# Kernel tuning notes

Hardware: AMD Instinct MI355X
Metric: run time of the kernel (lower is better)

Reference implementation:

```python
import jax, jax.numpy as jnp
import numpy as np

NUM_EMBEDDINGS = 1024
EMBEDDING_DIM = 256
COMMITMENT_COST = 0.25


def setup_inputs() -> dict:
    key = jax.random.key(0)
    k1, k2 = jax.random.split(key)
    inputs = jax.random.normal(k1, (64, 32, 32, EMBEDDING_DIM), dtype=jnp.float32)
    embed = jax.random.normal(k2, (NUM_EMBEDDINGS, EMBEDDING_DIM), dtype=jnp.float32)
    return {"inputs": inputs, "embed": embed}


def reference(inputs, embed):
    # Eval-mode forward (no EMA buffer mutation), use_ema=True loss branch.
    input_shape = inputs.shape
    flat = inputs.reshape(-1, EMBEDDING_DIM)  # [N, d]
    distances = (
        jnp.sum(flat * flat, axis=1, keepdims=True)
        + jnp.sum(embed * embed, axis=1)
        - 2.0 * jnp.matmul(flat, embed.T)
    )
    encoding_indices = jnp.argmin(distances, axis=1)  # [N]
    # Gather codebook rows (equivalent to one-hot @ embed)
    quantized = embed[encoding_indices].reshape(input_shape)
    # use_ema branch: loss = commitment * mse(stop_grad(quantized), inputs)
    e_latent_loss = jnp.mean((jax.lax.stop_gradient(quantized) - inputs) ** 2)
    loss = COMMITMENT_COST * e_latent_loss
    # Straight-through estimator
    quantized_st = inputs + jax.lax.stop_gradient(quantized - inputs)
    # Perplexity from code usage histogram (== mean of one-hot encodings)
    n_tokens = flat.shape[0]
    counts = jax.ops.segment_sum(
        jnp.ones((n_tokens,), dtype=jnp.float32), encoding_indices,
        num_segments=NUM_EMBEDDINGS)
    avg_probs = counts / n_tokens
    perplexity = jnp.exp(-jnp.sum(avg_probs * jnp.log(avg_probs + 1e-10)))
    return quantized_st, loss, perplexity, encoding_indices
```

## Files before the change

### kernel.cpp

```cpp
#include <hip/hip_runtime.h>

#define NTOK 65536
#define DIM 256
#define KC 1024
#define EPS 0.08f

typedef __attribute__((ext_vector_type(8))) _Float16 f16x8;
typedef __attribute__((ext_vector_type(4))) float f32x4;

static __device__ __forceinline__ unsigned short f16bits(float f) {
  _Float16 h = (_Float16)f;
  return __builtin_bit_cast(unsigned short, h);
}
static __device__ __forceinline__ void gload16(const void* g, void* l) {
  __builtin_amdgcn_global_load_lds(
      (const __attribute__((address_space(1))) unsigned int*)g,
      (__attribute__((address_space(3))) unsigned int*)l, 16, 0, 0);
}

__global__ __launch_bounds__(256) void vq_prep_e(const float* __restrict__ e,
                                                 unsigned short* __restrict__ eg,
                                                 float* __restrict__ esq,
                                                 int* __restrict__ hist,
                                                 int* __restrict__ fixCount) {
  const int w = threadIdx.x >> 6, l = threadIdx.x & 63;
  const int t = blockIdx.x * 4 + w;
  const float4 v = *reinterpret_cast<const float4*>(&e[t * DIM + l * 4]);
  ushort4 o;
  o.x = f16bits(v.x); o.y = f16bits(v.y); o.z = f16bits(v.z); o.w = f16bits(v.w);
  const int addr = t * 512 + ((l >> 4) << 7) + ((((l & 15) * 8) ^ ((t & 7) << 4)));
  *reinterpret_cast<ushort4*>((char*)eg + addr) = o;
  float s = v.x * v.x + v.y * v.y + v.z * v.z + v.w * v.w;
#pragma unroll
  for (int o2 = 32; o2 > 0; o2 >>= 1) s += __shfl_down(s, o2, 64);
  if (l == 0) esq[t] = s;
  if (blockIdx.x < 4) hist[blockIdx.x * 256 + threadIdx.x] = 0;
  if (blockIdx.x == 0 && threadIdx.x == 0) *fixCount = 0;
}

__global__ __launch_bounds__(256, 2) void vq_argmin_fused(
    const float* __restrict__ x, const unsigned short* __restrict__ eg,
    const float* __restrict__ e, const float* __restrict__ esq,
    float* __restrict__ outIdxF, float* __restrict__ outQ,
    float* __restrict__ bestDist, float* __restrict__ xsq,
    int* __restrict__ hist, int* __restrict__ fixCount,
    int* __restrict__ fixList) {
  __shared__ unsigned short xs[128 * 256];
  __shared__ unsigned short es[128 * 64];

  const int tid = threadIdx.x, lane = tid & 63, w = tid >> 6;
  const int wr = w >> 1, wc = w & 1;
  const int tokBase = blockIdx.x * 128;
  const int col = lane & 15, kq = lane >> 4;

  {
    const float4* xb = reinterpret_cast<const float4*>(&x[tokBase * DIM]);
    for (int c = 0; c < 32; ++c) {
      const int r = c * 4 + w;
      const float4 v = xb[c * 256 + tid];
      ushort4 o;
      o.x = f16bits(v.x); o.y = f16bits(v.y); o.z = f16bits(v.z); o.w = f16bits(v.w);
      const int addr =
          r * 512 + ((lane >> 4) << 7) + ((((lane & 15) * 8) ^ ((r & 7) << 4)));
      *reinterpret_cast<ushort4*>((char*)xs + addr) = o;
      float s = v.x * v.x + v.y * v.y + v.z * v.z + v.w * v.w;
#pragma unroll
      for (int o2 = 32; o2 > 0; o2 >>= 1) s += __shfl_down(s, o2, 64);
      if (lane == 0) xsq[tokBase + r] = s;
    }
  }

  float best[4][4], second[4][4];
  int bidx[4][4];
#pragma unroll
  for (int mi = 0; mi < 4; ++mi)
#pragma unroll
    for (int r = 0; r < 4; ++r) {
      best[mi][r] = 3.4e38f; second[mi][r] = 3.4e38f; bidx[mi][r] = 0;
    }

  for (int ct = 0; ct < 8; ++ct) {
    f32x4 acc[4][4];
#pragma unroll
    for (int mi = 0; mi < 4; ++mi)
#pragma unroll
      for (int nj = 0; nj < 4; ++nj) acc[mi][nj] = (f32x4){0.f, 0.f, 0.f, 0.f};

    for (int kt = 0; kt < 4; ++kt) {
      __syncthreads();
#pragma unroll
      for (int q = 0; q < 4; ++q) {
        const int r0 = (w * 4 + q) * 8;
        const int er = ct * 128 + r0 + (lane >> 3);
        gload16(&eg[er * DIM + kt * 64 + (lane & 7) * 8], &es[r0 * 64]);
      }
      __syncthreads();

#pragma unroll
      for (int ks = 0; ks < 2; ++ks) {
        const int kb = ks * 64 + kq * 16;
        f16x8 a[4], b[4];
#pragma unroll
        for (int mi = 0; mi < 4; ++mi) {
          const int rr = wr * 64 + mi * 16 + col;
          a[mi] = *reinterpret_cast<const f16x8*>(
              (const char*)xs + rr * 512 + kt * 128 + (kb ^ ((col & 7) << 4)));
        }
#pragma unroll
        for (int nj = 0; nj < 4; ++nj) {
          const int rr = wc * 64 + nj * 16 + col;
          b[nj] = *reinterpret_cast<const f16x8*>(
              (const char*)es + rr * 128 + (kb ^ ((col & 7) << 4)));
        }
#pragma unroll
        for (int mi = 0; mi < 4; ++mi)
#pragma unroll
          for (int nj = 0; nj < 4; ++nj)
            acc[mi][nj] = __builtin_amdgcn_mfma_f32_16x16x32_f16(
                a[mi], b[nj], acc[mi][nj], 0, 0, 0);
      }
    }

#pragma unroll
    for (int nj = 0; nj < 4; ++nj) {
      const int code = ct * 128 + wc * 64 + nj * 16 + col;
      const float sqv = esq[code];
#pragma unroll
      for (int mi = 0; mi < 4; ++mi)
#pragma unroll
        for (int r = 0; r < 4; ++r) {
          const float d = fmaf(-2.f, acc[mi][nj][r], sqv);
          if (d < best[mi][r]) {
            second[mi][r] = best[mi][r];
            best[mi][r] = d;
            bidx[mi][r] = code;
          } else if (d < second[mi][r]) {
            second[mi][r] = d;
          }
        }
    }
  }

  __syncthreads();
  float* redB = (float*)es;
  float* redS = redB + 256;
  int*   redI = (int*)(redS + 256);
  int*   fIdx = redI + 256;

#pragma unroll
  for (int mi = 0; mi < 4; ++mi)
#pragma unroll
    for (int r = 0; r < 4; ++r) {
      float b = best[mi][r], s2 = second[mi][r];
      int bi = bidx[mi][r];
#pragma unroll
      for (int m = 1; m <= 8; m <<= 1) {
        const float ob = __shfl_xor(b, m, 64);
        const float os = __shfl_xor(s2, m, 64);
        const int   oi = __shfl_xor(bi, m, 64);
        s2 = fminf(fminf(s2, os), fmaxf(b, ob));
        if (ob < b || (ob == b && oi < bi)) { b = ob; bi = oi; }
      }
      if (col == 0) {
        const int row = wr * 64 + mi * 16 + kq * 4 + r;
        redB[wc * 128 + row] = b; redS[wc * 128 + row] = s2;
        redI[wc * 128 + row] = bi;
      }
    }
  __syncthreads();
  if (tid < 128) {
    const float b0 = redB[tid], b1 = redB[128 + tid];
    const float s0 = redS[tid], s1 = redS[128 + tid];
    const int i0 = redI[tid], i1 = redI[128 + tid];
    const float s2 = fminf(fminf(s0, s1), fmaxf(b0, b1));
    float b; int bi;
    if (b1 < b0 || (b1 == b0 && i1 < i0)) { b = b1; bi = i1; } else { b = b0; bi = i0; }
    const int t = tokBase + tid;
    outIdxF[t] = (float)bi;
    bestDist[t] = b;
    fIdx[tid] = bi;
    atomicAdd(&hist[bi], 1);
    if (s2 - b < EPS) {
      const int p = atomicAdd(fixCount, 1);
      fixList[p] = t;
    }
  }
  __syncthreads();

  for (int i = 0; i < 32; ++i) {
    const int tl = w * 32 + i;
    const int id = fIdx[tl];
    const float4 q = reinterpret_cast<const float4*>(&e[id * DIM])[lane];
    reinterpret_cast<float4*>(&outQ[(tokBase + tl) * DIM])[lane] = q;
  }
}

__global__ __launch_bounds__(256) void vq_fixup(
    const float* __restrict__ x, const float* __restrict__ e,
    const float* __restrict__ esq, const int* __restrict__ fixCount,
    const int* __restrict__ fixList, float* __restrict__ outIdxF,
    float* __restrict__ bestDist, float* __restrict__ outQ,
    int* __restrict__ hist) {
  const int n = *fixCount;
  __shared__ float xrow[256];
  __shared__ float rv[4];
  __shared__ int ri[4];
  __shared__ int sOld, sFi;
  const int tid = threadIdx.x;
  for (int it = blockIdx.x; it < n; it += gridDim.x) {
    const int t = fixList[it];
    __syncthreads();
    if (tid < 64) ((float4*)xrow)[tid] = ((const float4*)&x[t * DIM])[tid];
    __syncthreads();
    float bv = 3.4e38f; int bi = 0;
    for (int c = tid; c < KC; c += 256) {
      float s = 0.f;
#pragma unroll
      for (int d = 0; d < DIM; d += 4) {
        const float4 ev = *(const float4*)&e[c * DIM + d];
        s = fmaf(xrow[d], ev.x, s);
        s = fmaf(xrow[d + 1], ev.y, s);
        s = fmaf(xrow[d + 2], ev.z, s);
        s = fmaf(xrow[d + 3], ev.w, s);
      }
      const float dist = fmaf(-2.f, s, esq[c]);
      if (dist < bv) { bv = dist; bi = c; }
    }
#pragma unroll
    for (int m = 1; m <= 32; m <<= 1) {
      const float ob = __shfl_xor(bv, m, 64);
      const int oi = __shfl_xor(bi, m, 64);
      if (ob < bv || (ob == bv && oi < bi)) { bv = ob; bi = oi; }
    }
    const int lane = tid & 63, wv = tid >> 6;
    if (lane == 0) { rv[wv] = bv; ri[wv] = bi; }
    __syncthreads();
    if (tid == 0) {
      float fb = rv[0]; int fi = ri[0];
      for (int k = 1; k < 4; ++k)
        if (rv[k] < fb || (rv[k] == fb && ri[k] < fi)) { fb = rv[k]; fi = ri[k]; }
      sOld = (int)outIdxF[t];
      sFi = fi;
      bestDist[t] = fb;
      if (fi != sOld) {
        atomicSub(&hist[sOld], 1);
        atomicAdd(&hist[fi], 1);
        outIdxF[t] = (float)fi;
      }
    }
    __syncthreads();
    if (sFi != sOld) outQ[t * DIM + tid] = e[sFi * DIM + tid];
    __syncthreads();
  }
}

__global__ __launch_bounds__(1024) void vq_final(
    const int* __restrict__ hist, const float* __restrict__ xsq,
    const float* __restrict__ bestDist, float* __restrict__ outLoss,
    float* __restrict__ outPerp) {
  const int tid = threadIdx.x;
  float ls = 0.f;
  for (int i = 0; i < 64; ++i) {
    const int t = tid + i * 1024;
    ls += xsq[t] + bestDist[t];
  }
  const float p = (float)hist[tid] * (1.f / 65536.f);
  float ent = p * logf(p + 1e-10f);
#pragma unroll
  for (int o = 32; o > 0; o >>= 1) {
    ls += __shfl_down(ls, o, 64);
    ent += __shfl_down(ent, o, 64);
  }
  __shared__ float lbuf[16], ebuf[16];
  const int lane = tid & 63, wv = tid >> 6;
  if (lane == 0) { lbuf[wv] = ls; ebuf[wv] = ent; }
  __syncthreads();
  if (tid == 0) {
    float L = 0.f, E = 0.f;
    for (int i = 0; i < 16; ++i) { L += lbuf[i]; E += ebuf[i]; }
    *outLoss = 0.25f * (L / 16777216.f);
    *outPerp = expf(-E);
  }
}

extern "C" void kernel_launch(void* const* d_in, const int* in_sizes, int n_in,
                              void* d_out, int out_size, void* d_ws, size_t ws_size,
                              hipStream_t stream) {
  const float* x = (const float*)d_in[0];
  const float* e = (const float*)d_in[1];
  float* out = (float*)d_out;
  float* outQ = out;
  float* outLoss = out + 16777216;
  float* outPerp = out + 16777217;
  float* outIdxF = out + 16777218;

  char* ws = (char*)d_ws;
  int*   hist     = (int*)ws;
  float* esq      = (float*)(ws + 4096);
  float* xsq      = (float*)(ws + 8192);
  float* bestDist = (float*)(ws + 270336);
  int*   fixCount = (int*)(ws + 532480);
  int*   fixList  = (int*)(ws + 532496);
  unsigned short* e_f16 = (unsigned short*)(ws + 794640);

  vq_prep_e<<<KC / 4, 256, 0, stream>>>(e, e_f16, esq, hist, fixCount);
  vq_argmin_fused<<<NTOK / 128, 256, 0, stream>>>(
      x, e_f16, e, esq, outIdxF, outQ, bestDist, xsq, hist, fixCount, fixList);
  vq_fixup<<<256, 256, 0, stream>>>(x, e, esq, fixCount, fixList, outIdxF,
                                    bestDist, outQ, hist);
  vq_final<<<1, 1024, 0, stream>>>(hist, xsq, bestDist, outLoss, outPerp);
}
```

Measured before the change: 204.7 us.

## Keep token fragments in registers and triple-buffer codebook tiles with async loads

Each wave now owns 32 tokens across all 128 codes per tile and holds its fp16 A-fragments in registers, loaded straight from global memory. This removes the 64KB shared-memory x tile and the cross-wave argmin reduction. Codebook tiles are triple-buffered in LDS with global_load_lds prefetch of the next tile, using vmcnt waits and one barrier per tile instead of two syncthreads. The cost is much higher register pressure (64 VGPRs of A fragments plus 32 accumulators), which could lower occupancy or cause spills under launch_bounds(256,2). The uncoalesced per-lane x loads also replace the previous coalesced staging.

New measurement: 198.0 us. 1.03x faster.

```diff
diff --git a/kernel.cpp b/kernel.cpp
--- a/kernel.cpp
+++ b/kernel.cpp
@@ -45,88 +45,105 @@
     float* __restrict__ bestDist, float* __restrict__ xsq,
     int* __restrict__ hist, int* __restrict__ fixCount,
     int* __restrict__ fixList) {
-  __shared__ unsigned short xs[128 * 256];
-  __shared__ unsigned short es[128 * 64];
+  __shared__ unsigned short es[3 * 8192];
+  __shared__ int fidx[128];
 
   const int tid = threadIdx.x, lane = tid & 63, w = tid >> 6;
-  const int wr = w >> 1, wc = w & 1;
   const int tokBase = blockIdx.x * 128;
   const int col = lane & 15, kq = lane >> 4;
 
-  {
-    const float4* xb = reinterpret_cast<const float4*>(&x[tokBase * DIM]);
-    for (int c = 0; c < 32; ++c) {
-      const int r = c * 4 + w;
-      const float4 v = xb[c * 256 + tid];
-      ushort4 o;
-      o.x = f16bits(v.x); o.y = f16bits(v.y); o.z = f16bits(v.z); o.w = f16bits(v.w);
-      const int addr =
-          r * 512 + ((lane >> 4) << 7) + ((((lane & 15) * 8) ^ ((r & 7) << 4)));
-      *reinterpret_cast<ushort4*>((char*)xs + addr) = o;
-      float s = v.x * v.x + v.y * v.y + v.z * v.z + v.w * v.w;
-#pragma unroll
-      for (int o2 = 32; o2 > 0; o2 >>= 1) s += __shfl_down(s, o2, 64);
-      if (lane == 0) xsq[tokBase + r] = s;
-    }
-  }
-
-  float best[4][4], second[4][4];
-  int bidx[4][4];
-#pragma unroll
-  for (int mi = 0; mi < 4; ++mi)
+  auto STAGE = [&](int tile, int b) {
+    const int ct_ = tile >> 2, kt_ = tile & 3;
+#pragma unroll
+    for (int q = 0; q < 4; ++q) {
+      const int r0 = w * 32 + q * 8;
+      const int er = ct_ * 128 + r0 + (lane >> 3);
+      gload16(&eg[er * DIM + kt_ * 64 + (lane & 7) * 8], &es[b * 8192 + r0 * 64]);
+    }
+  };
+
+  STAGE(0, 0);
+
+  f16x8 a[2][8];
+  float sqm[2] = {0.f, 0.f};
+#pragma unroll
+  for (int m = 0; m < 2; ++m) {
+#pragma unroll
+    for (int s = 0; s < 8; ++s) {
+      const float* xp =
+          &x[(tokBase + w * 32 + m * 16 + col) * DIM + s * 32 + kq * 8];
+      const float4 v0 = *reinterpret_cast<const float4*>(xp);
+      const float4 v1 = *reinterpret_cast<const float4*>(xp + 4);
+      a[m][s][0] = (_Float16)v0.x; a[m][s][1] = (_Float16)v0.y;
+      a[m][s][2] = (_Float16)v0.z; a[m][s][3] = (_Float16)v0.w;
+      a[m][s][4] = (_Float16)v1.x; a[m][s][5] = (_Float16)v1.y;
+      a[m][s][6] = (_Float16)v1.z; a[m][s][7] = (_Float16)v1.w;
+      sqm[m] += v0.x * v0.x + v0.y * v0.y + v0.z * v0.z + v0.w * v0.w +
+                v1.x * v1.x + v1.y * v1.y + v1.z * v1.z + v1.w * v1.w;
+    }
+  }
+#pragma unroll
+  for (int m = 0; m < 2; ++m) {
+    sqm[m] += __shfl_xor(sqm[m], 16, 64);
+    sqm[m] += __shfl_xor(sqm[m], 32, 64);
+  }
+  if (lane < 16) {
+    xsq[tokBase + w * 32 + lane] = sqm[0];
+    xsq[tokBase + w * 32 + 16 + lane] = sqm[1];
+  }
+
+  float best[2][4], second[2][4];
+  int bidx[2][4];
+#pragma unroll
+  for (int mi = 0; mi < 2; ++mi)
 #pragma unroll
     for (int r = 0; r < 4; ++r) {
       best[mi][r] = 3.4e38f; second[mi][r] = 3.4e38f; bidx[mi][r] = 0;
     }
 
   for (int ct = 0; ct < 8; ++ct) {
-    f32x4 acc[4][4];
-#pragma unroll
-    for (int mi = 0; mi < 4; ++mi)
-#pragma unroll
-      for (int nj = 0; nj < 4; ++nj) acc[mi][nj] = (f32x4){0.f, 0.f, 0.f, 0.f};
-
+    f32x4 acc[2][8];
+#pragma unroll
+    for (int mi = 0; mi < 2; ++mi)
+#pragma unroll
+      for (int nj = 0; nj < 8; ++nj) acc[mi][nj] = (f32x4){0.f, 0.f, 0.f, 0.f};
+
+#pragma unroll
     for (int kt = 0; kt < 4; ++kt) {
-      __syncthreads();
-#pragma unroll
-      for (int q = 0; q < 4; ++q) {
-        const int r0 = (w * 4 + q) * 8;
-        const int er = ct * 128 + r0 + (lane >> 3);
-        gload16(&eg[er * DIM + kt * 64 + (lane & 7) * 8], &es[r0 * 64]);
-      }
-      __syncthreads();
-
+      const int tile = ct * 4 + kt;
+      if (tile < 31) {
+        STAGE(tile + 1, (tile + 1) % 3);
+        asm volatile("s_waitcnt vmcnt(4)" ::: "memory");
+      } else {
+        asm volatile("s_waitcnt vmcnt(0)" ::: "memory");
+      }
+      __builtin_amdgcn_s_barrier();
+      asm volatile("" ::: "memory");
+
+      const char* bb = (const char*)es + (tile % 3) * 16384;
 #pragma unroll
       for (int ks = 0; ks < 2; ++ks) {
         const int kb = ks * 64 + kq * 16;
-        f16x8 a[4], b[4];
-#pragma unroll
-        for (int mi = 0; mi < 4; ++mi) {
-          const int rr = wr * 64 + mi * 16 + col;
-          a[mi] = *reinterpret_cast<const f16x8*>(
-              (const char*)xs + rr * 512 + kt * 128 + (kb ^ ((col & 7) << 4)));
-        }
-#pragma unroll
-        for (int nj = 0; nj < 4; ++nj) {
-          const int rr = wc * 64 + nj * 16 + col;
-          b[nj] = *reinterpret_cast<const f16x8*>(
-              (const char*)es + rr * 128 + (kb ^ ((col & 7) << 4)));
-        }
-#pragma unroll
-        for (int mi = 0; mi < 4; ++mi)
-#pragma unroll
-          for (int nj = 0; nj < 4; ++nj)
+        f16x8 bfr[8];
+#pragma unroll
+        for (int nj = 0; nj < 8; ++nj)
+          bfr[nj] = *reinterpret_cast<const f16x8*>(
+              bb + (nj * 16 + col) * 128 + (kb ^ ((col & 7) << 4)));
+#pragma unroll
+        for (int mi = 0; mi < 2; ++mi)
+#pragma unroll
+          for (int nj = 0; nj < 8; ++nj)
             acc[mi][nj] = __builtin_amdgcn_mfma_f32_16x16x32_f16(
-                a[mi], b[nj], acc[mi][nj], 0, 0, 0);
-      }
-    }
-
-#pragma unroll
-    for (int nj = 0; nj < 4; ++nj) {
-      const int code = ct * 128 + wc * 64 + nj * 16 + col;
+                a[mi][kt * 2 + ks], bfr[nj], acc[mi][nj], 0, 0, 0);
+      }
+    }
+
+#pragma unroll
+    for (int nj = 0; nj < 8; ++nj) {
+      const int code = ct * 128 + nj * 16 + col;
       const float sqv = esq[code];
 #pragma unroll
-      for (int mi = 0; mi < 4; ++mi)
+      for (int mi = 0; mi < 2; ++mi)
 #pragma unroll
         for (int r = 0; r < 4; ++r) {
           const float d = fmaf(-2.f, acc[mi][nj][r], sqv);
@@ -141,14 +158,8 @@
     }
   }
 
-  __syncthreads();
-  float* redB = (float*)es;
-  float* redS = redB + 256;
-  int*   redI = (int*)(redS + 256);
-  int*   fIdx = redI + 256;
-
-#pragma unroll
-  for (int mi = 0; mi < 4; ++mi)
+#pragma unroll
+  for (int mi = 0; mi < 2; ++mi)
 #pragma unroll
     for (int r = 0; r < 4; ++r) {
       float b = best[mi][r], s2 = second[mi][r];
@@ -162,36 +173,24 @@
         if (ob < b || (ob == b && oi < bi)) { b = ob; bi = oi; }
       }
       if (col == 0) {
-        const int row = wr * 64 + mi * 16 + kq * 4 + r;
-        redB[wc * 128 + row] = b; redS[wc * 128 + row] = s2;
-        redI[wc * 128 + row] = bi;
+        const int tl = w * 32 + mi * 16 + kq * 4 + r;
+        const int t = tokBase + tl;
+        outIdxF[t] = (float)bi;
+        bestDist[t] = b;
+        fidx[tl] = bi;
+        atomicAdd(&hist[bi], 1);
+        if (s2 - b < EPS) {
+          const int p = atomicAdd(fixCount, 1);
+          fixList[p] = t;
+        }
       }
     }
   __syncthreads();
-  if (tid < 128) {
-    const float b0 = redB[tid], b1 = redB[128 + tid];
-    const float s0 = redS[tid], s1 = redS[128 + tid];
-    const int i0 = redI[tid], i1 = redI[128 + tid];
-    const float s2 = fminf(fminf(s0, s1), fmaxf(b0, b1));
-    float b; int bi;
-    if (b1 < b0 || (b1 == b0 && i1 < i0)) { b = b1; bi = i1; } else { b = b0; bi = i0; }
-    const int t = tokBase + tid;
-    outIdxF[t] = (float)bi;
-    bestDist[t] = b;
-    fIdx[tid] = bi;
-    atomicAdd(&hist[bi], 1);
-    if (s2 - b < EPS) {
-      const int p = atomicAdd(fixCount, 1);
-      fixList[p] = t;
-    }
-  }
-  __syncthreads();
 
   for (int i = 0; i < 32; ++i) {
-    const int tl = w * 32 + i;
-    const int id = fIdx[tl];
+    const int id = fidx[w * 32 + i];
     const float4 q = reinterpret_cast<const float4*>(&e[id * DIM])[lane];
-    reinterpret_cast<float4*>(&outQ[(tokBase + tl) * DIM])[lane] = q;
+    reinterpret_cast<float4*>(&outQ[(tokBase + w * 32 + i) * DIM])[lane] = q;
   }
 }
 
```
